# Optimization experiments

Hardware: AMD Instinct MI355X
Metric: run time of the kernel (lower is better)

The kernel has to match this reference:

```python
import jax, jax.numpy as jnp
import numpy as np

RADIUS = [3, 3, 4, 4]
DILATION = [1, 2, 1, 2]
N_HEAD = 4
D_K = 8
SCALE = 1.0 / np.sqrt(8.0)  # module hardcodes sqrt(8)


def _patches(a, r, d):
    # a: (b, t, c, h, w) -> (b, t, c, ls2, h, w), dilated (2r+1)x(2r+1) window,
    # zero padding (invalid positions masked separately).
    b, t, c, h, w = a.shape
    p = r * d
    ap = jnp.pad(a, ((0, 0), (0, 0), (0, 0), (p, p), (p, p)))
    ls = 2 * r + 1
    sl = [ap[..., dy * d:dy * d + h, dx * d:dx * d + w]
          for dy in range(ls) for dx in range(ls)]
    return jnp.stack(sl, axis=3)


def _valid_mask(h, w, r, d):
    # (ls2, h, w) bool: True where window position is inside the image
    m = _patches(jnp.ones((1, 1, 1, h, w)), r, d)
    return m[0, 0, 0] > 0.5


def _head_attn(q, k, v, r, d):
    # q,k,v: (b, t, c, h, w); attention over all t' frames x local window
    b, t, c, h, w = q.shape
    kp = _patches(k, r, d)        # (b, t', c, p, h, w)
    vp = _patches(v, r, d)
    valid = _valid_mask(h, w, r, d)  # (p, h, w)
    e = jnp.einsum('btchw,bscphw->btsphw', q, kp) * SCALE
    e = jnp.where(valid[None, None, None], e, -jnp.inf)  # OOB -> -inf like CUDA kernel
    e = e.reshape(b, t, t * valid.shape[0], h, w)
    attn = jax.nn.softmax(e, axis=2).reshape(b, t, t, -1, h, w)
    return jnp.einsum('btsphw,bscphw->btchw', attn, vp)


def setup_inputs() -> dict:
    key = jax.random.key(0)
    kx, kq, kk, kv, ko = jax.random.split(key, 5)
    C = 32
    std = 1.0 / np.sqrt(C)
    x = jax.random.normal(kx, (2, 5, C, 64, 64), dtype=jnp.float32)
    Wq = jax.random.normal(kq, (N_HEAD * D_K, C), dtype=jnp.float32) * std
    Wk = jax.random.normal(kk, (N_HEAD * D_K, C), dtype=jnp.float32) * std
    Wv = jax.random.normal(kv, (N_HEAD * D_K, C), dtype=jnp.float32) * std
    Wo = jax.random.normal(ko, (C, C), dtype=jnp.float32) * std
    return {"x": x, "Wq": Wq, "Wk": Wk, "Wv": Wv, "Wo": Wo}


def reference(x, Wq, Wk, Wv, Wo):
    # 1x1x1 Conv3d == per-pixel channel matmul
    q = jnp.einsum('btchw,kc->btkhw', x, Wq)
    k = jnp.einsum('btchw,kc->btkhw', x, Wk)
    v = jnp.einsum('btchw,kc->btkhw', x, Wv)
    outs = []
    for i in range(N_HEAD):
        s = slice(i * D_K, (i + 1) * D_K)
        outs.append(_head_attn(q[:, :, s], k[:, :, s], v[:, :, s],
                               RADIUS[i], DILATION[i]))
    out = jnp.concatenate(outs, axis=2)
    out = jnp.einsum('btchw,kc->btkhw', out, Wo)
    return out + x
```

## Files before the change

### kernel.cpp

```cpp
#include <hip/hip_runtime.h>
#include <stdint.h>

#define NT 5
#define NC 32
#define NH 4
#define HW 4096
#define NPIX 40960
#define QS 0.51006972789f
#define EBIAS 12.0f
#define NINF (-__builtin_inff())

typedef _Float16 half_t;
typedef half_t h2 __attribute__((ext_vector_type(2)));

static __device__ __forceinline__ h2 as_h2(uint32_t u) {
  union { uint32_t u; h2 h; } c; c.u = u; return c.h;
}
static __device__ __forceinline__ uint32_t pack_h2(float a, float b) {
  union { h2 h; uint32_t u; } c;
  c.h.x = (half_t)a; c.h.y = (half_t)b;
  return c.u;
}

#if __has_builtin(__builtin_amdgcn_exp2f)
#define EXP2(x) __builtin_amdgcn_exp2f(x)
#else
#define EXP2(x) exp2f(x)
#endif

static __device__ __forceinline__ float dot8i(const uint4& a, const uint4& b, float c) {
#if __has_builtin(__builtin_amdgcn_fdot2)
  c = __builtin_amdgcn_fdot2(as_h2(a.x), as_h2(b.x), c, false);
  c = __builtin_amdgcn_fdot2(as_h2(a.y), as_h2(b.y), c, false);
  c = __builtin_amdgcn_fdot2(as_h2(a.z), as_h2(b.z), c, false);
  c = __builtin_amdgcn_fdot2(as_h2(a.w), as_h2(b.w), c, false);
  return c;
#else
  const h2 a0 = as_h2(a.x), a1 = as_h2(a.y), a2 = as_h2(a.z), a3 = as_h2(a.w);
  const h2 b0 = as_h2(b.x), b1 = as_h2(b.y), b2 = as_h2(b.z), b3 = as_h2(b.w);
  c = fmaf((float)a0.x, (float)b0.x, c);
  c = fmaf((float)a0.y, (float)b0.y, c);
  c = fmaf((float)a1.x, (float)b1.x, c);
  c = fmaf((float)a1.y, (float)b1.y, c);
  c = fmaf((float)a2.x, (float)b2.x, c);
  c = fmaf((float)a2.y, (float)b2.y, c);
  c = fmaf((float)a3.x, (float)b3.x, c);
  c = fmaf((float)a3.y, (float)b3.y, c);
  return c;
#endif
}

__global__ __launch_bounds__(256) void qkv_kernel(
    const float* __restrict__ x,
    const float* __restrict__ Wq, const float* __restrict__ Wk,
    const float* __restrict__ Wv,
    uint2* __restrict__ qf, uint2* __restrict__ kf, uint2* __restrict__ vf)
{
  const int p   = blockIdx.x * 256 + threadIdx.x;
  const int by  = blockIdx.y;
  const int h   = by >> 1;
  const int jg  = by & 1;
  const int bt  = p >> 12;
  const int pix = p & 4095;

  const float* xp = x + (size_t)bt * (NC * HW) + pix;
  float xc[NC];
  #pragma unroll
  for (int c = 0; c < NC; ++c) xc[c] = xp[(size_t)c * HW];

  float qv[4], kv4[4], vv4[4];
  #pragma unroll
  for (int j = 0; j < 4; ++j) {
    const int o = h * 8 + jg * 4 + j;
    float aq = 0.f, ak = 0.f, av = 0.f;
    #pragma unroll
    for (int c = 0; c < NC; ++c) {
      const float xv = xc[c];
      aq = fmaf(xv, Wq[o * NC + c], aq);
      ak = fmaf(xv, Wk[o * NC + c], ak);
      av = fmaf(xv, Wv[o * NC + c], av);
    }
    qv[j] = aq * QS; kv4[j] = ak; vv4[j] = av;
  }
  const size_t base = (((size_t)bt * NH + h) * HW + pix) * 2 + jg;
  uint2 qq, kk, vv;
  qq.x = pack_h2(qv[0], qv[1]);  qq.y = pack_h2(qv[2], qv[3]);
  kk.x = pack_h2(kv4[0], kv4[1]); kk.y = pack_h2(kv4[2], kv4[3]);
  vv.x = pack_h2(vv4[0], vv4[1]); vv.y = pack_h2(vv4[2], vv4[3]);
  qf[base] = qq;
  kf[base] = kk;
  vf[base] = vv;
}

template <int R, int D>
static __device__ __forceinline__ void attn_body(
    int b, int t, int h, int s, int yb,
    const uint4* __restrict__ qf, const uint4* __restrict__ kf,
    const uint4* __restrict__ vf,
    uint4* __restrict__ pa, float* __restrict__ pl,
    uint4* __restrict__ k_lds, uint4* __restrict__ v_lds)
{
  constexpr int LS    = 2 * R + 1;
  constexpr int NROWS = 8 + 2 * R;
  const int tid  = threadIdx.x;
  const int w    = tid >> 6;
  const int lane = tid & 63;

  const int y0 = (D == 1) ? (yb * 8) : ((yb & 1) + 2 * ((yb >> 1) * 8));

  const uint4* kg = kf + (size_t)((b * NT + s) * NH + h) * HW;
  const uint4* vg = vf + (size_t)((b * NT + s) * NH + h) * HW;
  for (int idx = tid; idx < NROWS * 64; idx += 256) {
    const int r  = idx >> 6, xs = idx & 63;
    int ys = y0 + (r - R) * D;
    ys = ys < 0 ? 0 : (ys > 63 ? 63 : ys);
    const int pos = (D == 1) ? xs : ((xs & 1) * 32 + (xs >> 1));
    k_lds[r * 64 + pos] = kg[ys * 64 + xs];
    v_lds[r * 64 + pos] = vg[ys * 64 + xs];
  }
  __syncthreads();

  const int xp = lane >> 5;
  const int cb = (D == 1) ? lane : (lane & 31);
  const int x  = (D == 1) ? lane : (2 * (lane & 31) + xp);
  const int yA = y0 + 2 * w * D;
  const int yB = yA + D;
  const int pixA = yA * 64 + x, pixB = yB * 64 + x;

  const uint4* qp = qf + (size_t)((b * NT + t) * NH + h) * HW;
  const uint4 qA = qp[pixA];
  const uint4 qB = qp[pixB];

  float lA = 0.f, lB = 0.f;
  h2 aA[4], aB[4];
  const h2 z2 = { (half_t)0.f, (half_t)0.f };
  #pragma unroll
  for (int i = 0; i < 4; ++i) { aA[i] = z2; aB[i] = z2; }

  #pragma unroll 2
  for (int u = 0; u <= LS; ++u) {
    const bool okA = (u < LS) && ((unsigned)(yA + (u - R) * D) < 64u);
    const bool okB = (u > 0)  && ((unsigned)(yB + (u - 1 - R) * D) < 64u);
    if (!(okA || okB)) continue;
    const float biA = okA ? -EBIAS : NINF;
    const float biB = okB ? -EBIAS : NINF;
    const uint4* kr = k_lds + (2 * w + u) * 64;
    const uint4* vr = v_lds + (2 * w + u) * 64;
    #pragma unroll
    for (int dx = -R; dx <= R; ++dx) {
      const int  cx  = cb + dx;
      const bool okx = (unsigned)cx < (D == 1 ? 64u : 32u);
      const int  cc  = okx ? cx : 0;
      const int  pos = (D == 1) ? cc : (xp * 32 + cc);
      const uint4 kk = kr[pos];
      const uint4 vv = vr[pos];
      const h2 w0 = as_h2(vv.x), w1 = as_h2(vv.y), w2 = as_h2(vv.z), w3 = as_h2(vv.w);
      const float eo = okx ? 0.f : NINF;
      const float pA = EXP2(dot8i(qA, kk, biA + eo));
      const float pB = EXP2(dot8i(qB, kk, biB + eo));
      lA += pA; lB += pB;
      const half_t pAh = (half_t)pA, pBh = (half_t)pB;
      const h2 pA2 = { pAh, pAh }, pB2 = { pBh, pBh };
      aA[0] += pA2 * w0; aA[1] += pA2 * w1; aA[2] += pA2 * w2; aA[3] += pA2 * w3;
      aB[0] += pB2 * w0; aB[1] += pB2 * w1; aB[2] += pB2 * w2; aB[3] += pB2 * w3;
    }
  }

  const size_t plane = (size_t)(s * NH + h) * NPIX + (size_t)(b * NT + t) * HW;
  union { h2 hh[4]; uint4 u; } cA, cB;
  #pragma unroll
  for (int i = 0; i < 4; ++i) { cA.hh[i] = aA[i]; cB.hh[i] = aB[i]; }
  pa[plane + pixA] = cA.u;
  pa[plane + pixB] = cB.u;
  pl[plane + pixA] = lA;
  pl[plane + pixB] = lB;
}

__global__ __launch_bounds__(256) void attn_kernel(
    const uint4* __restrict__ qf, const uint4* __restrict__ kf,
    const uint4* __restrict__ vf, uint4* __restrict__ pa, float* __restrict__ pl)
{
  __shared__ uint4 k_lds[16 * 64];
  __shared__ uint4 v_lds[16 * 64];
  const int bid = blockIdx.x;
  const int h   = bid & 3;
  int r = bid >> 2;
  const int yb = r & 7; r >>= 3;
  const int s  = r % 5;
  const int bt = r / 5;
  const int t = bt % NT, b = bt / NT;
  if      (h == 0) attn_body<3, 1>(b, t, 0, s, yb, qf, kf, vf, pa, pl, k_lds, v_lds);
  else if (h == 1) attn_body<3, 2>(b, t, 1, s, yb, qf, kf, vf, pa, pl, k_lds, v_lds);
  else if (h == 2) attn_body<4, 1>(b, t, 2, s, yb, qf, kf, vf, pa, pl, k_lds, v_lds);
  else             attn_body<4, 2>(b, t, 3, s, yb, qf, kf, vf, pa, pl, k_lds, v_lds);
}

__global__ __launch_bounds__(256) void proj_kernel(
    const uint4* __restrict__ pa, const float* __restrict__ pl,
    const float* __restrict__ x, const float* __restrict__ Wo,
    float* __restrict__ out)
{
  const int p   = blockIdx.x * 256 + threadIdx.x;
  const int og  = blockIdx.y;
  const int bt  = p >> 12;
  const int pix = p & 4095;

  float oc[32];
  #pragma unroll
  for (int h = 0; h < NH; ++h) {
    float a[8], l = 0.f;
    #pragma unroll
    for (int i = 0; i < 8; ++i) a[i] = 0.f;
    #pragma unroll
    for (int s = 0; s < NT; ++s) {
      const size_t plane = (size_t)(s * NH + h) * NPIX + p;
      const uint4 v = pa[plane];
      l += pl[plane];
      const h2 v0 = as_h2(v.x), v1 = as_h2(v.y), v2 = as_h2(v.z), v3 = as_h2(v.w);
      a[0] += (float)v0.x; a[1] += (float)v0.y;
      a[2] += (float)v1.x; a[3] += (float)v1.y;
      a[4] += (float)v2.x; a[5] += (float)v2.y;
      a[6] += (float)v3.x; a[7] += (float)v3.y;
    }
    const float inv = 1.0f / l;
    #pragma unroll
    for (int i = 0; i < 8; ++i) oc[h * 8 + i] = a[i] * inv;
  }

  const float* xpt = x + (size_t)bt * (NC * HW) + pix;
  float* yp = out + (size_t)bt * (NC * HW) + pix;
  #pragma unroll
  for (int oo = 0; oo < 8; ++oo) {
    const int o = og * 8 + oo;
    float acc = xpt[(size_t)o * HW];
    #pragma unroll
    for (int c = 0; c < NC; ++c)
      acc = fmaf(oc[c], Wo[o * NC + c], acc);
    yp[(size_t)o * HW] = acc;
  }
}

extern "C" void kernel_launch(void* const* d_in, const int* in_sizes, int n_in,
                              void* d_out, int out_size, void* d_ws, size_t ws_size,
                              hipStream_t stream)
{
  const float* x  = (const float*)d_in[0];
  const float* Wq = (const float*)d_in[1];
  const float* Wk = (const float*)d_in[2];
  const float* Wv = (const float*)d_in[3];
  const float* Wo = (const float*)d_in[4];

  char* ws = (char*)d_ws;
  uint2* qf = (uint2*)ws;
  uint2* kf = (uint2*)(ws + 2621440);
  uint2* vf = (uint2*)(ws + 2 * 2621440);
  uint4* pa = (uint4*)(ws + 3 * 2621440);
  float* pl = (float*)(ws + 3 * 2621440 + 13107200);

  qkv_kernel<<<dim3(160, 8), 256, 0, stream>>>(x, Wq, Wk, Wv, qf, kf, vf);
  attn_kernel<<<1600, 256, 0, stream>>>((const uint4*)qf, (const uint4*)kf,
                                        (const uint4*)vf, pa, pl);
  proj_kernel<<<dim3(160, 4), 256, 0, stream>>>(pa, pl, x, Wo, (float*)d_out);
}
```

Before: 117.6 us.

## Process all query frames per block to reuse each staged key/value window

```diff
diff --git a/kernel.cpp b/kernel.cpp
--- a/kernel.cpp
+++ b/kernel.cpp
@@ -94,23 +94,23 @@
 
 template <int R, int D>
 static __device__ __forceinline__ void attn_body(
-    int b, int t, int h, int s, int yb,
+    int b, int h, int s, int yb,
     const uint4* __restrict__ qf, const uint4* __restrict__ kf,
     const uint4* __restrict__ vf,
     uint4* __restrict__ pa, float* __restrict__ pl,
     uint4* __restrict__ k_lds, uint4* __restrict__ v_lds)
 {
   constexpr int LS    = 2 * R + 1;
-  constexpr int NROWS = 8 + 2 * R;
+  constexpr int NROWS = 4 + 2 * R;
   const int tid  = threadIdx.x;
   const int w    = tid >> 6;
   const int lane = tid & 63;
 
-  const int y0 = (D == 1) ? (yb * 8) : ((yb & 1) + 2 * ((yb >> 1) * 8));
+  const int y0 = (D == 1) ? (yb * 4) : ((yb & 1) + 2 * ((yb >> 1) * 4));
 
   const uint4* kg = kf + (size_t)((b * NT + s) * NH + h) * HW;
   const uint4* vg = vf + (size_t)((b * NT + s) * NH + h) * HW;
-  for (int idx = tid; idx < NROWS * 64; idx += 256) {
+  for (int idx = tid; idx < NROWS * 64; idx += 128) {
     const int r  = idx >> 6, xs = idx & 63;
     int ys = y0 + (r - R) * D;
     ys = ys < 0 ? 0 : (ys > 63 ? 63 : ys);
@@ -127,17 +127,25 @@
   const int yB = yA + D;
   const int pixA = yA * 64 + x, pixB = yB * 64 + x;
 
-  const uint4* qp = qf + (size_t)((b * NT + t) * NH + h) * HW;
-  const uint4 qA = qp[pixA];
-  const uint4 qB = qp[pixB];
-
-  float lA = 0.f, lB = 0.f;
-  h2 aA[4], aB[4];
+  uint4 qA[NT], qB[NT];
+  #pragma unroll
+  for (int t = 0; t < NT; ++t) {
+    const uint4* qp = qf + (size_t)((b * NT + t) * NH + h) * HW;
+    qA[t] = qp[pixA];
+    qB[t] = qp[pixB];
+  }
+
+  float lA[NT], lB[NT];
+  h2 aA[NT][4], aB[NT][4];
   const h2 z2 = { (half_t)0.f, (half_t)0.f };
   #pragma unroll
-  for (int i = 0; i < 4; ++i) { aA[i] = z2; aB[i] = z2; }
-
-  #pragma unroll 2
+  for (int t = 0; t < NT; ++t) {
+    lA[t] = 0.f; lB[t] = 0.f;
+    #pragma unroll
+    for (int i = 0; i < 4; ++i) { aA[t][i] = z2; aB[t][i] = z2; }
+  }
+
+  #pragma unroll 1
   for (int u = 0; u <= LS; ++u) {
     const bool okA = (u < LS) && ((unsigned)(yA + (u - R) * D) < 64u);
     const bool okB = (u > 0)  && ((unsigned)(yB + (u - 1 - R) * D) < 64u);
@@ -156,43 +164,51 @@
       const uint4 vv = vr[pos];
       const h2 w0 = as_h2(vv.x), w1 = as_h2(vv.y), w2 = as_h2(vv.z), w3 = as_h2(vv.w);
       const float eo = okx ? 0.f : NINF;
-      const float pA = EXP2(dot8i(qA, kk, biA + eo));
-      const float pB = EXP2(dot8i(qB, kk, biB + eo));
-      lA += pA; lB += pB;
-      const half_t pAh = (half_t)pA, pBh = (half_t)pB;
-      const h2 pA2 = { pAh, pAh }, pB2 = { pBh, pBh };
-      aA[0] += pA2 * w0; aA[1] += pA2 * w1; aA[2] += pA2 * w2; aA[3] += pA2 * w3;
-      aB[0] += pB2 * w0; aB[1] += pB2 * w1; aB[2] += pB2 * w2; aB[3] += pB2 * w3;
+      const float bA = biA + eo, bB = biB + eo;
+      #pragma unroll
+      for (int t = 0; t < NT; ++t) {
+        const float pA = EXP2(dot8i(qA[t], kk, bA));
+        const float pB = EXP2(dot8i(qB[t], kk, bB));
+        lA[t] += pA; lB[t] += pB;
+        const half_t pAh = (half_t)pA, pBh = (half_t)pB;
+        const h2 pA2 = { pAh, pAh }, pB2 = { pBh, pBh };
+        aA[t][0] += pA2 * w0; aA[t][1] += pA2 * w1;
+        aA[t][2] += pA2 * w2; aA[t][3] += pA2 * w3;
+        aB[t][0] += pB2 * w0; aB[t][1] += pB2 * w1;
+        aB[t][2] += pB2 * w2; aB[t][3] += pB2 * w3;
+      }
     }
   }
 
-  const size_t plane = (size_t)(s * NH + h) * NPIX + (size_t)(b * NT + t) * HW;
-  union { h2 hh[4]; uint4 u; } cA, cB;
-  #pragma unroll
-  for (int i = 0; i < 4; ++i) { cA.hh[i] = aA[i]; cB.hh[i] = aB[i]; }
-  pa[plane + pixA] = cA.u;
-  pa[plane + pixB] = cB.u;
-  pl[plane + pixA] = lA;
-  pl[plane + pixB] = lB;
-}
-
-__global__ __launch_bounds__(256) void attn_kernel(
+  #pragma unroll
+  for (int t = 0; t < NT; ++t) {
+    const size_t plane = (size_t)(s * NH + h) * NPIX + (size_t)(b * NT + t) * HW;
+    union { h2 hh[4]; uint4 u; } cA, cB;
+    #pragma unroll
+    for (int i = 0; i < 4; ++i) { cA.hh[i] = aA[t][i]; cB.hh[i] = aB[t][i]; }
+    pa[plane + pixA] = cA.u;
+    pa[plane + pixB] = cB.u;
+    pl[plane + pixA] = lA[t];
+    pl[plane + pixB] = lB[t];
+  }
+}
+
+__global__ __launch_bounds__(128, 3) void attn_kernel(
     const uint4* __restrict__ qf, const uint4* __restrict__ kf,
     const uint4* __restrict__ vf, uint4* __restrict__ pa, float* __restrict__ pl)
 {
-  __shared__ uint4 k_lds[16 * 64];
-  __shared__ uint4 v_lds[16 * 64];
+  __shared__ uint4 k_lds[12 * 64];
+  __shared__ uint4 v_lds[12 * 64];
   const int bid = blockIdx.x;
   const int h   = bid & 3;
   int r = bid >> 2;
-  const int yb = r & 7; r >>= 3;
+  const int yb = r & 15; r >>= 4;
   const int s  = r % 5;
-  const int bt = r / 5;
-  const int t = bt % NT, b = bt / NT;
-  if      (h == 0) attn_body<3, 1>(b, t, 0, s, yb, qf, kf, vf, pa, pl, k_lds, v_lds);
-  else if (h == 1) attn_body<3, 2>(b, t, 1, s, yb, qf, kf, vf, pa, pl, k_lds, v_lds);
-  else if (h == 2) attn_body<4, 1>(b, t, 2, s, yb, qf, kf, vf, pa, pl, k_lds, v_lds);
-  else             attn_body<4, 2>(b, t, 3, s, yb, qf, kf, vf, pa, pl, k_lds, v_lds);
+  const int b  = r / 5;
+  if      (h == 0) attn_body<3, 1>(b, 0, s, yb, qf, kf, vf, pa, pl, k_lds, v_lds);
+  else if (h == 1) attn_body<3, 2>(b, 1, s, yb, qf, kf, vf, pa, pl, k_lds, v_lds);
+  else if (h == 2) attn_body<4, 1>(b, 2, s, yb, qf, kf, vf, pa, pl, k_lds, v_lds);
+  else             attn_body<4, 2>(b, 3, s, yb, qf, kf, vf, pa, pl, k_lds, v_lds);
 }
 
 __global__ __launch_bounds__(256) void proj_kernel(
@@ -258,7 +274,7 @@
   float* pl = (float*)(ws + 3 * 2621440 + 13107200);
 
   qkv_kernel<<<dim3(160, 8), 256, 0, stream>>>(x, Wq, Wk, Wv, qf, kf, vf);
-  attn_kernel<<<1600, 256, 0, stream>>>((const uint4*)qf, (const uint4*)kf,
-                                        (const uint4*)vf, pa, pl);
+  attn_kernel<<<640, 128, 0, stream>>>((const uint4*)qf, (const uint4*)kf,
+                                       (const uint4*)vf, pa, pl);
   proj_kernel<<<dim3(160, 4), 256, 0, stream>>>(pa, pl, x, Wo, (float*)d_out);
 }
```

Result: slower. 159.2 us (+35.4%).
